# Performance work log

Hardware: AMD Instinct MI355X
Metric: run time of the kernel (lower is better)

Reference implementation:

```python
import jax, jax.numpy as jnp
import numpy as np

N = 1_000_000   # total nodes
B = 1024        # number of graphs
H = 64          # node feature dim / LSTM hidden
STEPS = 5       # Set2Set processing steps
PROJ = 128      # projection_dim


def setup_inputs() -> dict:
    key = jax.random.key(0)
    ks = jax.random.split(key, 12)
    x = jax.random.normal(ks[0], (N, H), dtype=jnp.float32)
    batch = jnp.sort(jax.random.randint(ks[1], (N,), 0, B)).astype(jnp.int64)
    s = 1.0 / np.sqrt(H)
    # torch.nn.LSTM(input_size=2H, hidden_size=H), gate order i,f,g,o
    W_ih = jax.random.uniform(ks[2], (4 * H, 2 * H), minval=-s, maxval=s, dtype=jnp.float32)
    W_hh = jax.random.uniform(ks[3], (4 * H, H), minval=-s, maxval=s, dtype=jnp.float32)
    b_ih = jax.random.uniform(ks[4], (4 * H,), minval=-s, maxval=s, dtype=jnp.float32)
    b_hh = jax.random.uniform(ks[5], (4 * H,), minval=-s, maxval=s, dtype=jnp.float32)
    s1 = 1.0 / np.sqrt(2 * H)
    W1 = jax.random.uniform(ks[6], (256, 2 * H), minval=-s1, maxval=s1, dtype=jnp.float32)
    b1 = jax.random.uniform(ks[7], (256,), minval=-s1, maxval=s1, dtype=jnp.float32)
    s2 = 1.0 / np.sqrt(256)
    W2 = jax.random.uniform(ks[8], (PROJ, 256), minval=-s2, maxval=s2, dtype=jnp.float32)
    b2 = jax.random.uniform(ks[9], (PROJ,), minval=-s2, maxval=s2, dtype=jnp.float32)
    return {"x": x, "batch": batch, "W_ih": W_ih, "W_hh": W_hh, "b_ih": b_ih,
            "b_hh": b_hh, "W1": W1, "b1": b1, "W2": W2, "b2": b2}


def _set2set(x, batch, W_ih, W_hh, b_ih, b_hh):
    q_star = jnp.zeros((B, 2 * H), x.dtype)
    h = jnp.zeros((B, H), x.dtype)
    c = jnp.zeros((B, H), x.dtype)
    for _ in range(STEPS):
        gates = q_star @ W_ih.T + b_ih + h @ W_hh.T + b_hh
        i, f, g, o = jnp.split(gates, 4, axis=-1)
        i = jax.nn.sigmoid(i); f = jax.nn.sigmoid(f)
        g = jnp.tanh(g); o = jax.nn.sigmoid(o)
        c = f * c + i * g
        h = o * jnp.tanh(c)
        q = h  # [B, H]
        # segment-wise attention over ragged node sets
        e = jnp.sum(x * q[batch], axis=-1)                         # [N]
        emax = jax.ops.segment_max(e, batch, num_segments=B)       # [B]
        a = jnp.exp(e - emax[batch])
        denom = jax.ops.segment_sum(a, batch, num_segments=B)
        a = a / jnp.maximum(denom, 1e-16)[batch]
        r = jax.ops.segment_sum(a[:, None] * x, batch, num_segments=B)  # [B, H]
        q_star = jnp.concatenate([q, r], axis=-1)
    return q_star


def reference(x, batch, W_ih, W_hh, b_ih, b_hh, W1, b1, W2, b2):
    out = _set2set(x, batch, W_ih, W_hh, b_ih, b_hh)   # [B, 2H]
    out = out @ W1.T + b1                               # [B, 256]
    out = jax.nn.relu(out) @ W2.T + b2                  # [B, PROJ]
    return out
```

## Files before the change

### kernel.cpp

```cpp
#include <hip/hip_runtime.h>
#include <float.h>
#include <math.h>

#define NB 1024
#define HD 64
#define NSTEPS 5
#define RT 9

__device__ __forceinline__ float sigmoidf_(float x) {
    return 1.0f / (1.0f + __expf(-x));
}

__global__ void seg_bounds_kernel(const int* __restrict__ batch,
                                  int* __restrict__ seg_start, int n) {
    int i = blockIdx.x * blockDim.x + threadIdx.x;
    if (i >= n) return;
    int b = batch[i];
    if (i == 0) {
        for (int j = 0; j <= b; ++j) seg_start[j] = 0;
    } else {
        int pb = batch[i - 1];
        for (int j = pb + 1; j <= b; ++j) seg_start[j] = i;
    }
    if (i == n - 1) {
        for (int j = b + 1; j <= NB; ++j) seg_start[j] = n;
    }
}

#define ONLINE_UPD(U, XV, NODE)                                         \
    {                                                                   \
        float d = (XV).x * q4.x;                                        \
        d = fmaf((XV).y, q4.y, d);                                      \
        d = fmaf((XV).z, q4.z, d);                                      \
        d = fmaf((XV).w, q4.w, d);                                      \
        d += __shfl_xor(d, 1);                                          \
        d += __shfl_xor(d, 2);                                          \
        d += __shfl_xor(d, 4);                                          \
        d += __shfl_xor(d, 8);                                          \
        bool valid = (NODE) < len;                                      \
        float eeff = valid ? d : -FLT_MAX;                              \
        float nm = fmaxf(mm[U], eeff);                                  \
        float sc = __expf(mm[U] - nm);                                  \
        float w = valid ? __expf(eeff - nm) : 0.0f;                     \
        ss[U] = fmaf(ss[U], sc, w);                                     \
        rr[U].x = fmaf(rr[U].x, sc, w * (XV).x);                        \
        rr[U].y = fmaf(rr[U].y, sc, w * (XV).y);                        \
        rr[U].z = fmaf(rr[U].z, sc, w * (XV).z);                        \
        rr[U].w = fmaf(rr[U].w, sc, w * (XV).w);                        \
        mm[U] = nm;                                                     \
    }

__global__ __launch_bounds__(512) void set2set_fused_kernel(
    const float* __restrict__ x,
    const int* __restrict__ seg,
    const float* __restrict__ W_ih,
    const float* __restrict__ W_hh,
    const float* __restrict__ b_ih,
    const float* __restrict__ b_hh,
    const float* __restrict__ W1,
    const float* __restrict__ b1,
    const float* __restrict__ W2,
    const float* __restrict__ b2,
    float* __restrict__ out)
{
    __shared__ __align__(16) float hs[HD], cs[HD], rs[HD];
    __shared__ __align__(16) float gates[256], gpart[256];
    __shared__ __align__(16) float lr[8][HD];
    __shared__ float lm[8], ls[8];

    const int b = blockIdx.x;
    const int tid = threadIdx.x;
    const int lane = tid & 63;
    const int wv = tid >> 6;
    const int fc = lane & 15;
    const int grp = lane >> 4;

    const int s0 = seg[b], e0 = seg[b + 1];
    const int len = e0 - s0;
    const int ntiles = (len + 15) >> 4;
    const int maxidx4 = e0 * 16 - 1;

    float4 xr[4 * RT];
#pragma unroll
    for (int j = 0; j < RT; ++j) {
        int t = wv + 8 * j;
        if (t < ntiles) {
            int tb4 = (s0 + t * 16) * 16;
#pragma unroll
            for (int u = 0; u < 4; ++u) {
                int g4 = min(tb4 + u * 64 + lane, maxidx4);
                xr[4 * j + u] = *(const float4*)(x + (size_t)g4 * 4);
            }
        }
    }

    if (tid < HD) { hs[tid] = 0.0f; cs[tid] = 0.0f; rs[tid] = 0.0f; }
    __syncthreads();

    for (int step = 0; step < NSTEPS; ++step) {
        if (step == 0) {
            if (tid < 256) gates[tid] = b_ih[tid] + b_hh[tid];
        } else {
            float acc = 0.0f;
            if (tid < 256) {
                acc = b_ih[tid] + b_hh[tid];
                const float4* w = (const float4*)(W_ih + tid * 128);
                const float4* hq = (const float4*)hs;
                const float4* rq = (const float4*)rs;
#pragma unroll
                for (int k = 0; k < 16; ++k) {
                    float4 ww = w[k]; float4 v = hq[k];
                    acc = fmaf(ww.x, v.x, acc); acc = fmaf(ww.y, v.y, acc);
                    acc = fmaf(ww.z, v.z, acc); acc = fmaf(ww.w, v.w, acc);
                }
#pragma unroll
                for (int k = 0; k < 16; ++k) {
                    float4 ww = w[16 + k]; float4 v = rq[k];
                    acc = fmaf(ww.x, v.x, acc); acc = fmaf(ww.y, v.y, acc);
                    acc = fmaf(ww.z, v.z, acc); acc = fmaf(ww.w, v.w, acc);
                }
            } else {
                int j = tid - 256;
                float a2 = 0.0f;
                const float4* w = (const float4*)(W_hh + j * 64);
                const float4* hq = (const float4*)hs;
#pragma unroll
                for (int k = 0; k < 16; ++k) {
                    float4 ww = w[k]; float4 v = hq[k];
                    a2 = fmaf(ww.x, v.x, a2); a2 = fmaf(ww.y, v.y, a2);
                    a2 = fmaf(ww.z, v.z, a2); a2 = fmaf(ww.w, v.w, a2);
                }
                gpart[j] = a2;
            }
            __syncthreads();
            if (tid < 256) gates[tid] = acc + gpart[tid];
        }
        __syncthreads();

        if (tid < HD) {
            float ig = sigmoidf_(gates[tid]);
            float fg = sigmoidf_(gates[tid + 64]);
            float gg = tanhf(gates[tid + 128]);
            float og = sigmoidf_(gates[tid + 192]);
            float cp = (step == 0) ? 0.0f : cs[tid];
            float cn = fmaf(fg, cp, ig * gg);
            cs[tid] = cn;
            hs[tid] = og * tanhf(cn);
        }
        __syncthreads();

        float4 q4 = *(const float4*)(hs + fc * 4);
        float mm[4], ss[4];
        float4 rr[4];
#pragma unroll
        for (int u = 0; u < 4; ++u) {
            mm[u] = -FLT_MAX; ss[u] = 0.0f;
            rr[u] = make_float4(0.0f, 0.0f, 0.0f, 0.0f);
        }

#pragma unroll
        for (int j = 0; j < RT; ++j) {
            int t = wv + 8 * j;
            if (t < ntiles) {
                int nbase = t * 16;
                ONLINE_UPD(0, xr[4 * j + 0], nbase + 0 * 4 + grp);
                ONLINE_UPD(1, xr[4 * j + 1], nbase + 1 * 4 + grp);
                ONLINE_UPD(2, xr[4 * j + 2], nbase + 2 * 4 + grp);
                ONLINE_UPD(3, xr[4 * j + 3], nbase + 3 * 4 + grp);
            }
        }
        for (int t = 8 * RT + wv; t < ntiles; t += 8) {
            int tb4 = (s0 + t * 16) * 16;
            int nbase = t * 16;
#pragma unroll
            for (int u = 0; u < 4; ++u) {
                int g4 = min(tb4 + u * 64 + lane, maxidx4);
                float4 xv = *(const float4*)(x + (size_t)g4 * 4);
                ONLINE_UPD(u, xv, nbase + u * 4 + grp);
            }
        }

        float m = mm[0], sum = ss[0];
        float4 r4 = rr[0];
#pragma unroll
        for (int u = 1; u < 4; ++u) {
            float nm = fmaxf(m, mm[u]);
            float s1 = __expf(m - nm);
            float s2 = __expf(mm[u] - nm);
            sum = sum * s1 + ss[u] * s2;
            r4.x = r4.x * s1 + rr[u].x * s2;
            r4.y = r4.y * s1 + rr[u].y * s2;
            r4.z = r4.z * s1 + rr[u].z * s2;
            r4.w = r4.w * s1 + rr[u].w * s2;
            m = nm;
        }
#pragma unroll
        for (int off = 16; off < 64; off <<= 1) {
            float om = __shfl_xor(m, off);
            float os = __shfl_xor(sum, off);
            float ox = __shfl_xor(r4.x, off);
            float oy = __shfl_xor(r4.y, off);
            float oz = __shfl_xor(r4.z, off);
            float ow = __shfl_xor(r4.w, off);
            float nm = fmaxf(m, om);
            float s1 = __expf(m - nm);
            float s2 = __expf(om - nm);
            sum = sum * s1 + os * s2;
            r4.x = r4.x * s1 + ox * s2;
            r4.y = r4.y * s1 + oy * s2;
            r4.z = r4.z * s1 + oz * s2;
            r4.w = r4.w * s1 + ow * s2;
            m = nm;
        }
        if (lane < 16) {
            if (lane == 0) { lm[wv] = m; ls[wv] = sum; }
            *(float4*)&lr[wv][lane * 4] = r4;
        }
        __syncthreads();

        if (tid < HD) {
            float M = lm[0];
#pragma unroll
            for (int w = 1; w < 8; ++w) M = fmaxf(M, lm[w]);
            float S = 0.0f, rf = 0.0f;
#pragma unroll
            for (int w = 0; w < 8; ++w) {
                float ww = __expf(lm[w] - M);
                S = fmaf(ls[w], ww, S);
                rf = fmaf(lr[w][tid], ww, rf);
            }
            rs[tid] = rf / fmaxf(S, 1e-16f);
        }
        __syncthreads();
    }

    if (tid < 256) {
        float acc = b1[tid];
        const float4* w = (const float4*)(W1 + tid * 128);
        const float4* hq = (const float4*)hs;
        const float4* rq = (const float4*)rs;
#pragma unroll
        for (int k = 0; k < 16; ++k) {
            float4 ww = w[k]; float4 v = hq[k];
            acc = fmaf(ww.x, v.x, acc); acc = fmaf(ww.y, v.y, acc);
            acc = fmaf(ww.z, v.z, acc); acc = fmaf(ww.w, v.w, acc);
        }
#pragma unroll
        for (int k = 0; k < 16; ++k) {
            float4 ww = w[16 + k]; float4 v = rq[k];
            acc = fmaf(ww.x, v.x, acc); acc = fmaf(ww.y, v.y, acc);
            acc = fmaf(ww.z, v.z, acc); acc = fmaf(ww.w, v.w, acc);
        }
        gates[tid] = fmaxf(acc, 0.0f);
    }
    __syncthreads();
    if (tid < 128) {
        float acc = b2[tid];
        const float4* w = (const float4*)(W2 + tid * 256);
        const float4* hq = (const float4*)gates;
#pragma unroll 8
        for (int k = 0; k < 64; ++k) {
            float4 ww = w[k]; float4 v = hq[k];
            acc = fmaf(ww.x, v.x, acc); acc = fmaf(ww.y, v.y, acc);
            acc = fmaf(ww.z, v.z, acc); acc = fmaf(ww.w, v.w, acc);
        }
        out[b * 128 + tid] = acc;
    }
}

extern "C" void kernel_launch(void* const* d_in, const int* in_sizes, int n_in,
                              void* d_out, int out_size, void* d_ws, size_t ws_size,
                              hipStream_t stream) {
    const float* x     = (const float*)d_in[0];
    const int*   batch = (const int*)d_in[1];
    const float* W_ih  = (const float*)d_in[2];
    const float* W_hh  = (const float*)d_in[3];
    const float* b_ih  = (const float*)d_in[4];
    const float* b_hh  = (const float*)d_in[5];
    const float* W1    = (const float*)d_in[6];
    const float* b1    = (const float*)d_in[7];
    const float* W2    = (const float*)d_in[8];
    const float* b2    = (const float*)d_in[9];
    float* out = (float*)d_out;
    const int N = in_sizes[1];

    int* seg = (int*)d_ws;

    seg_bounds_kernel<<<(N + 255) / 256, 256, 0, stream>>>(batch, seg, N);
    set2set_fused_kernel<<<NB, 512, 0, stream>>>(x, seg, W_ih, W_hh, b_ih, b_hh,
                                                 W1, b1, W2, b2, out);
}
```

Before: 598.5 us.

## Stage most of each segment's node features in LDS via async global-to-LDS loads

Replaces the large per-thread register cache of node tiles with a 36-tile LDS buffer filled by asynchronous global_load_lds, keeping a smaller register cache for the next tiles. The cached data is reused across all five Set2Set steps without re-reading HBM. It aims to cut register pressure and extend the cached fraction of each segment, at the cost of LDS read latency and nearly the full LDS capacity. It also pins waves-per-EU to 2.

```diff
diff --git a/kernel.cpp b/kernel.cpp
--- a/kernel.cpp
+++ b/kernel.cpp
@@ -5,7 +5,8 @@
 #define NB 1024
 #define HD 64
 #define NSTEPS 5
-#define RT 9
+#define LT 36
+#define RT2 4
 
 __device__ __forceinline__ float sigmoidf_(float x) {
     return 1.0f / (1.0f + __expf(-x));
@@ -25,6 +26,12 @@
     if (i == n - 1) {
         for (int j = b + 1; j <= NB; ++j) seg_start[j] = n;
     }
+}
+
+__device__ __forceinline__ void async_ld16(const float* g, float* l) {
+    __builtin_amdgcn_global_load_lds(
+        (const __attribute__((address_space(1))) void*)g,
+        (__attribute__((address_space(3))) void*)l, 16, 0, 0);
 }
 
 #define ONLINE_UPD(U, XV, NODE)                                         \
@@ -50,7 +57,9 @@
         mm[U] = nm;                                                     \
     }
 
-__global__ __launch_bounds__(512) void set2set_fused_kernel(
+__global__ __attribute__((amdgpu_flat_work_group_size(512, 512)))
+__attribute__((amdgpu_waves_per_eu(2, 2)))
+void set2set_fused_kernel(
     const float* __restrict__ x,
     const int* __restrict__ seg,
     const float* __restrict__ W_ih,
@@ -63,6 +72,7 @@
     const float* __restrict__ b2,
     float* __restrict__ out)
 {
+    __shared__ __align__(16) float xl[LT * 16 * HD];
     __shared__ __align__(16) float hs[HD], cs[HD], rs[HD];
     __shared__ __align__(16) float gates[256], gpart[256];
     __shared__ __align__(16) float lr[8][HD];
@@ -78,12 +88,13 @@
     const int s0 = seg[b], e0 = seg[b + 1];
     const int len = e0 - s0;
     const int ntiles = (len + 15) >> 4;
-    const int maxidx4 = e0 * 16 - 1;
-
-    float4 xr[4 * RT];
-#pragma unroll
-    for (int j = 0; j < RT; ++j) {
-        int t = wv + 8 * j;
+    const int maxidx4 = max(e0 * 16 - 1, 0);
+    const int ltiles = min(LT, ntiles);
+
+    float4 xr[4 * RT2];
+#pragma unroll
+    for (int j = 0; j < RT2; ++j) {
+        int t = LT + wv + 8 * j;
         if (t < ntiles) {
             int tb4 = (s0 + t * 16) * 16;
 #pragma unroll
@@ -93,6 +104,16 @@
             }
         }
     }
+    for (int t = wv; t < ltiles; t += 8) {
+        int tb4 = (s0 + t * 16) * 16;
+        float* dst = xl + t * 1024;
+#pragma unroll
+        for (int u = 0; u < 4; ++u) {
+            int g4 = min(tb4 + u * 64 + lane, maxidx4);
+            async_ld16(x + (size_t)g4 * 4, dst + u * 256);
+        }
+    }
+    asm volatile("s_waitcnt vmcnt(0)" ::: "memory");
 
     if (tid < HD) { hs[tid] = 0.0f; cs[tid] = 0.0f; rs[tid] = 0.0f; }
     __syncthreads();
@@ -158,9 +179,18 @@
             rr[u] = make_float4(0.0f, 0.0f, 0.0f, 0.0f);
         }
 
-#pragma unroll
-        for (int j = 0; j < RT; ++j) {
-            int t = wv + 8 * j;
+        for (int t = wv; t < ltiles; t += 8) {
+            const float* bt = xl + t * 1024;
+            int nbase = t * 16;
+#pragma unroll
+            for (int u = 0; u < 4; ++u) {
+                float4 xv = *(const float4*)(bt + u * 256 + grp * 64 + fc * 4);
+                ONLINE_UPD(u, xv, nbase + u * 4 + grp);
+            }
+        }
+#pragma unroll
+        for (int j = 0; j < RT2; ++j) {
+            int t = LT + wv + 8 * j;
             if (t < ntiles) {
                 int nbase = t * 16;
                 ONLINE_UPD(0, xr[4 * j + 0], nbase + 0 * 4 + grp);
@@ -169,7 +199,7 @@
                 ONLINE_UPD(3, xr[4 * j + 3], nbase + 3 * 4 + grp);
             }
         }
-        for (int t = 8 * RT + wv; t < ntiles; t += 8) {
+        for (int t = LT + 8 * RT2 + wv; t < ntiles; t += 8) {
             int tb4 = (s0 + t * 16) * 16;
             int nbase = t * 16;
 #pragma unroll
```

Result: faster. 576.9 us (-3.6%).
